# Performance work log

Measured on AMD Instinct MI355X. Metric: run time of the kernel, lower is better.

## Reference

```python
import jax, jax.numpy as jnp
import numpy as np


def setup_inputs() -> dict:
    key = jax.random.key(0)
    k1, k2, k3, k4 = jax.random.split(key, 4)
    B, N, D = 4, 2048, 1024
    scale = 1.0 / np.sqrt(D)
    return {
        "x": jax.random.normal(k1, (B, N, D), dtype=jnp.float32),
        "Wq": jax.random.normal(k2, (D, D), dtype=jnp.float32) * scale,
        "Wk": jax.random.normal(k3, (D, D), dtype=jnp.float32) * scale,
        "Wv": jax.random.normal(k4, (D, D), dtype=jnp.float32) * scale,
    }


def reference(x, Wq, Wk, Wv):
    # x: [b, n, d_in]; W*: [d_out, d_in] (torch Linear convention y = x @ W.T)
    q = jnp.einsum("bnd,od->bno", x, Wq)
    k = jnp.einsum("bnd,od->bno", x, Wk)
    v = jnp.einsum("bnd,od->bno", x, Wv)
    n = x.shape[1]
    d_out = k.shape[-1]
    scores = jnp.einsum("bqd,bkd->bqk", q, k)  # [b, n, n]
    causal = jnp.triu(jnp.ones((n, n), dtype=bool), k=1)  # True above diagonal
    scores = jnp.where(causal[None, :, :], -jnp.inf, scores)
    # NOTE: faithful to source -- softmax over dim=1 (query axis), not dim=-1
    attn = jax.nn.softmax(scores / jnp.sqrt(jnp.float32(d_out)), axis=1)
    # dropout p=0.0 (eval): identity
    return jnp.einsum("bqk,bkd->bqd", attn, v)
```

## Files before the change

kernel.cpp:

```cpp
#include <hip/hip_runtime.h>
#include <stdint.h>
#include <math.h>


typedef __attribute__((ext_vector_type(8))) short short8;
typedef __attribute__((ext_vector_type(4))) float f32x4;

static __device__ __forceinline__ ushort f2bf(float f) {
  union { float f; uint32_t u; } v; v.f = f;
  uint32_t r = v.u + 0x7FFFu + ((v.u >> 16) & 1u);
  return (ushort)(r >> 16);
}
static __device__ __forceinline__ float bf2f(ushort u) {
  union { uint32_t u; float f; } v; v.u = ((uint32_t)u) << 16;
  return v.f;
}

static __device__ __forceinline__ void gload_lds16(const ushort* g, ushort* l) {
  __builtin_amdgcn_global_load_lds(
      (const __attribute__((address_space(1))) void*)g,
      (__attribute__((address_space(3))) void*)l, 16, 0, 0);
}

#define SBAR()   __builtin_amdgcn_s_barrier()
#define SCHED0() __builtin_amdgcn_sched_barrier(0)
#define WAITL0() do { asm volatile("s_waitcnt lgkmcnt(0)" ::: "memory"); SCHED0(); } while (0)
#define WAITV3() asm volatile("s_waitcnt vmcnt(3)" ::: "memory")
#define WAITV2() asm volatile("s_waitcnt vmcnt(2)" ::: "memory")
#define WAITV0() asm volatile("s_waitcnt vmcnt(0)" ::: "memory")

__global__ void cast_all(const float* __restrict__ x, const float* __restrict__ Wq,
                         const float* __restrict__ Wk, const float* __restrict__ Wv,
                         ushort* __restrict__ xb, ushort* __restrict__ Wb,
                         int n_x4, int n_w4) {
  int i = blockIdx.x * blockDim.x + threadIdx.x;
  const float* src; ushort* dst; int off;
  if (i < n_x4) { src = x; dst = xb; off = i; }
  else {
    int j = i - n_x4;
    int z = j / n_w4;
    off = j - z * n_w4;
    src = (z == 0) ? Wq : (z == 1) ? Wk : Wv;
    dst = Wb + (long)z * n_w4 * 4;
  }
  float4 v = ((const float4*)src)[off];
  ushort4 o;
  o.x = f2bf(v.x); o.y = f2bf(v.y); o.z = f2bf(v.z); o.w = f2bf(v.w);
  ((ushort4*)dst)[off] = o;
}

__global__ __launch_bounds__(512, 4) void proj_all(
    const ushort* __restrict__ xb, const ushort* __restrict__ Wb,
    ushort* __restrict__ QK, ushort* __restrict__ Vt)
{
  const int D = 1024;
  const long BND = 8388608;
  int L = blockIdx.x;
  L = (L & 7) * 96 + (L >> 3);

  const ushort* Ab; const ushort* Bb;
  int bm0, bn0;
  if (L < 512) {
    int rem = L & 255;
    bm0 = (rem >> 3) * 256;
    bn0 = (rem & 7) * 128;
    Ab = xb;
    Bb = Wb + (long)(L >> 8) * D * D;
  } else {
    int rem = L - 512;
    bm0 = (rem >> 6) * 256;
    bn0 = (rem & 63) * 128;
    Ab = Wb + 2L * D * D;
    Bb = xb;
  }

  const int nk = 32;

  __shared__ uint4 lds_v[73728 / 16];
  char* lds = (char*)lds_v;

  const int tid  = threadIdx.x;
  const int lane = tid & 63;
  const int wave = tid >> 6;
  const int wr   = wave >> 1;
  const int wc   = wave & 1;
  const int fr   = lane & 15;
  const int fg   = lane >> 4;

  f32x4 acc[4][4];
#pragma unroll
  for (int i = 0; i < 4; ++i)
#pragma unroll
    for (int j = 0; j < 4; ++j) acc[i][j] = (f32x4){0.f, 0.f, 0.f, 0.f};

  auto STAGE = [&](int tt) {
    if (tt >= nk) return;
    char* slab = lds + (tt % 3) * 24576;
#pragma unroll
    for (int u = 0; u < 2; ++u) {
      int s = u * 512 + tid;
      int row = s >> 2;
      int cc = (s & 3) ^ ((row >> 1) & 3);
      gload_lds16(Ab + (long)(bm0 + row) * D + tt * 32 + cc * 8,
                  (ushort*)(slab + s * 16));
    }
    {
      int s = tid;
      int row = s >> 2;
      int cc = (s & 3) ^ ((row >> 1) & 3);
      gload_lds16(Bb + (long)(bn0 + row) * D + tt * 32 + cc * 8,
                  (ushort*)(slab + 16384 + s * 16));
    }
  };

  STAGE(0); STAGE(1);
  WAITV3();
  SBAR();

  for (int t = 0; t < nk; ++t) {
    char* slab = lds + (t % 3) * 24576;
    STAGE(t + 2);

    short8 a[4], b[4];
#pragma unroll
    for (int i = 0; i < 4; ++i) {
      int row = wr * 64 + i * 16 + fr;
      int cc = fg ^ ((row >> 1) & 3);
      a[i] = *(const short8*)(slab + row * 64 + cc * 16);
    }
#pragma unroll
    for (int j = 0; j < 4; ++j) {
      int row = wc * 64 + j * 16 + fr;
      int cc = fg ^ ((row >> 1) & 3);
      b[j] = *(const short8*)(slab + 16384 + row * 64 + cc * 16);
    }
    WAITL0();
    __builtin_amdgcn_s_setprio(1);
#pragma unroll
    for (int i = 0; i < 4; ++i)
#pragma unroll
      for (int j = 0; j < 4; ++j)
        acc[i][j] = __builtin_amdgcn_mfma_f32_16x16x32_bf16(a[i], b[j], acc[i][j], 0, 0, 0);
    __builtin_amdgcn_s_setprio(0);

    if (t + 2 < nk) { WAITV3(); } else { WAITV0(); }
    SBAR();
  }

  if (L < 512) {
    ushort* Cb = QK + (long)(L >> 8) * BND;
#pragma unroll
    for (int i = 0; i < 4; ++i)
#pragma unroll
      for (int j = 0; j < 4; ++j)
#pragma unroll
        for (int r = 0; r < 4; ++r) {
          int row = bm0 + wr * 64 + i * 16 + fg * 4 + r;
          int col = bn0 + wc * 64 + j * 16 + fr;
          Cb[(long)row * D + col] = f2bf(acc[i][j][r]);
        }
  } else {
    ushort* Cb = Vt + (long)(bn0 >> 11) * D * 2048;
#pragma unroll
    for (int i = 0; i < 4; ++i)
#pragma unroll
      for (int j = 0; j < 4; ++j)
#pragma unroll
        for (int r = 0; r < 4; ++r) {
          int row = bm0 + wr * 64 + i * 16 + fg * 4 + r;
          int col = (bn0 + wc * 64 + j * 16 + fr) & 2047;
          Cb[(long)row * 2048 + col] = f2bf(acc[i][j][r]);
        }
  }
}

__global__ __launch_bounds__(512, 4) void gemm_s(
    const ushort* __restrict__ Q, const ushort* __restrict__ Kb, ushort* __restrict__ S,
    float* __restrict__ pMg, float* __restrict__ pZg)
{
  const int NQ = 2048, D = 1024;
  int bid = blockIdx.x;
  bid = (bid & 7) * 68 + (bid >> 3);
  const int b = bid / 136;
  int t = bid - b * 136;
  int i = (int)((sqrtf(8.f * t + 1.f) - 1.f) * 0.5f);
  while ((i + 1) * (i + 2) / 2 <= t) ++i;
  while (i * (i + 1) / 2 > t) --i;
  const int j = t - i * (i + 1) / 2;
  const int bm0 = i * 128;
  const int bn0 = j * 128;

  const ushort* Ab = Q + (long)b * NQ * D;
  const ushort* Bb = Kb + (long)b * NQ * D;

  const int nk = 32;

  __shared__ uint4 lds_v[49152 / 16];
  char* lds = (char*)lds_v;

  const int tid  = threadIdx.x;
  const int lane = tid & 63;
  const int wave = tid >> 6;
  const int wr   = wave >> 2;
  const int wc   = wave & 3;
  const int fr   = lane & 15;
  const int fg   = lane >> 4;

  f32x4 acc[4][2];
#pragma unroll
  for (int ii = 0; ii < 4; ++ii)
#pragma unroll
    for (int jj = 0; jj < 2; ++jj) acc[ii][jj] = (f32x4){0.f, 0.f, 0.f, 0.f};

  auto STAGE = [&](int tt) {
    if (tt >= nk) return;
    char* slab = lds + (tt % 3) * 16384;
    {
      int s = tid;
      int row = s >> 2;
      int cc = (s & 3) ^ ((row >> 1) & 3);
      gload_lds16(Ab + (long)(bm0 + row) * D + tt * 32 + cc * 8,
                  (ushort*)(slab + s * 16));
    }
    {
      int s = tid;
      int row = s >> 2;
      int cc = (s & 3) ^ ((row >> 1) & 3);
      gload_lds16(Bb + (long)(bn0 + row) * D + tt * 32 + cc * 8,
                  (ushort*)(slab + 8192 + s * 16));
    }
  };

  STAGE(0); STAGE(1);
  WAITV2();
  SBAR();

  for (int tt = 0; tt < nk; ++tt) {
    char* slab = lds + (tt % 3) * 16384;
    STAGE(tt + 2);

    short8 a[4], bf[2];
#pragma unroll
    for (int ii = 0; ii < 4; ++ii) {
      int row = wr * 64 + ii * 16 + fr;
      int cc = fg ^ ((row >> 1) & 3);
      a[ii] = *(const short8*)(slab + row * 64 + cc * 16);
    }
#pragma unroll
    for (int jj = 0; jj < 2; ++jj) {
      int row = wc * 32 + jj * 16 + fr;
      int cc = fg ^ ((row >> 1) & 3);
      bf[jj] = *(const short8*)(slab + 8192 + row * 64 + cc * 16);
    }
    WAITL0();
    __builtin_amdgcn_s_setprio(1);
#pragma unroll
    for (int ii = 0; ii < 4; ++ii)
#pragma unroll
      for (int jj = 0; jj < 2; ++jj)
        acc[ii][jj] = __builtin_amdgcn_mfma_f32_16x16x32_bf16(a[ii], bf[jj], acc[ii][jj], 0, 0, 0);
    __builtin_amdgcn_s_setprio(0);

    if (tt + 2 < nk) { WAITV2(); } else { WAITV0(); }
    SBAR();
  }

  ushort* Cb = S + (long)b * NQ * NQ;
  float mcol[2];
#pragma unroll
  for (int jj = 0; jj < 2; ++jj) {
    const int colg = bn0 + wc * 32 + jj * 16 + fr;
    float m = -3.0e38f;
#pragma unroll
    for (int ii = 0; ii < 4; ++ii)
#pragma unroll
      for (int r = 0; r < 4; ++r) {
        int rowg = bm0 + wr * 64 + ii * 16 + fg * 4 + r;
        float v = acc[ii][jj][r] * 0.03125f;
        acc[ii][jj][r] = v;
        Cb[(long)rowg * NQ + colg] = f2bf(v);
        m = (rowg >= colg) ? fmaxf(m, v) : m;
      }
    m = fmaxf(m, __shfl_xor(m, 16));
    m = fmaxf(m, __shfl_xor(m, 32));
    mcol[jj] = m;
  }
  float* red = (float*)lds;
  if (fg == 0) {
    red[wr * 128 + wc * 32 + fr]      = mcol[0];
    red[wr * 128 + wc * 32 + 16 + fr] = mcol[1];
  }
  SBAR();
  float Mf[2], zcol[2];
#pragma unroll
  for (int jj = 0; jj < 2; ++jj) {
    const int c = wc * 32 + jj * 16 + fr;
    Mf[jj] = fmaxf(red[c], red[128 + c]);
    const int colg = bn0 + c;
    float z = 0.f;
#pragma unroll
    for (int ii = 0; ii < 4; ++ii)
#pragma unroll
      for (int r = 0; r < 4; ++r) {
        int rowg = bm0 + wr * 64 + ii * 16 + fg * 4 + r;
        z += (rowg >= colg) ? __expf(acc[ii][jj][r] - Mf[jj]) : 0.f;
      }
    z += __shfl_xor(z, 16);
    z += __shfl_xor(z, 32);
    zcol[jj] = z;
  }
  if (fg == 0) {
    red[256 + wr * 128 + wc * 32 + fr]      = zcol[0];
    red[256 + wr * 128 + wc * 32 + 16 + fr] = zcol[1];
  }
  SBAR();
  if (wr == 0 && fg == 0) {
#pragma unroll
    for (int jj = 0; jj < 2; ++jj) {
      const int c = wc * 32 + jj * 16 + fr;
      long o = ((long)b * 16 + i) * NQ + bn0 + c;
      pMg[o] = Mf[jj];
      pZg[o] = red[256 + c] + red[256 + 128 + c];
    }
  }
}

__global__ void colstats_combine(const float* __restrict__ pM, const float* __restrict__ pZ,
                                 float2* __restrict__ Mz, int Nq) {
  int idx = blockIdx.x * 256 + threadIdx.x;
  int b = idx / Nq, k = idx - b * Nq;
  const int i0 = k >> 7;
  const float* PM = pM + (long)b * 16 * Nq + k;
  const float* PZ = pZ + (long)b * 16 * Nq + k;
  float M = -3.0e38f;
  for (int c = i0; c < 16; ++c) M = fmaxf(M, PM[(long)c * Nq]);
  float Z = 0.f;
  for (int c = i0; c < 16; ++c) Z += PZ[(long)c * Nq] * __expf(PM[(long)c * Nq] - M);
  Mz[idx] = make_float2(M, 1.0f / Z);
}

__global__ void make_p(ushort* __restrict__ S, const float2* __restrict__ Mz, int Nq) {
  long t = (long)blockIdx.x * 256 + threadIdx.x;
  int kb = (int)(t % (Nq / 8)) * 8;
  long row = t / (Nq / 8);
  int q = (int)(row % Nq);
  int b = (int)(row / Nq);
  int kend = ((q >> 7) + 1) << 7;
  if (kb >= kend) return;
  ushort* Sp = S + row * Nq + kb;
  union { uint4 v; ushort u[8]; } d, o;
  d.v = *(const uint4*)Sp;
  const float2* mz = Mz + (long)b * Nq + kb;
#pragma unroll
  for (int j = 0; j < 8; ++j) {
    float2 m = mz[j];
    float p = (q >= kb + j) ? __expf(bf2f(d.u[j]) - m.x) * m.y : 0.f;
    o.u[j] = f2bf(p);
  }
  *(uint4*)Sp = o.v;
}

__global__ __launch_bounds__(512, 4) void gemm_pv(
    const ushort* __restrict__ P, const ushort* __restrict__ Vt, float* __restrict__ out)
{
  const int NQ = 2048, DD = 1024;
  int L = blockIdx.x;
  L = (L & 7) * 64 + (L >> 3);
  const int pr = L & 7, dt = (L >> 3) & 15, b = L >> 7;

  const ushort* Pb = P + (long)b * NQ * NQ;
  const ushort* Vb = Vt + (long)b * DD * NQ + (long)(dt * 64) * NQ;
  float* Ob = out + (long)b * NQ * DD;

  __shared__ uint4 lds_v[73728 / 16];
  char* lds = (char*)lds_v;

  const int tid  = threadIdx.x;
  const int lane = tid & 63;
  const int wave = tid >> 6;
  const int wr   = wave >> 1;
  const int wc   = wave & 1;
  const int fr   = lane & 15;
  const int fg   = lane >> 4;

  for (int h = 0; h < 2; ++h) {
    const int tq = h ? (15 - pr) : pr;
    const int q0 = tq * 128;
    const ushort* Aq = Pb + (long)q0 * NQ;
    const int nk = (tq + 1) * 2;

    f32x4 acc[2][2];
#pragma unroll
    for (int i = 0; i < 2; ++i)
#pragma unroll
      for (int j = 0; j < 2; ++j) acc[i][j] = (f32x4){0.f, 0.f, 0.f, 0.f};

    auto STAGE = [&](int tt) {
      if (tt >= nk) return;
      char* slab = lds + (tt % 3) * 24576;
#pragma unroll
      for (int u = 0; u < 2; ++u) {
        int s = u * 512 + tid;
        int row = s >> 3;
        int cc = (s & 7) ^ (row & 7);
        gload_lds16(Aq + (long)row * NQ + tt * 64 + cc * 8,
                    (ushort*)(slab + s * 16));
      }
      {
        int s = tid;
        int row = s >> 3;
        int cc = (s & 7) ^ (row & 7);
        gload_lds16(Vb + (long)row * NQ + tt * 64 + cc * 8,
                    (ushort*)(slab + 16384 + s * 16));
      }
    };

    STAGE(0); STAGE(1);
    WAITV3();
    SBAR();

    for (int t = 0; t < nk; ++t) {
      char* slab = lds + (t % 3) * 24576;
      STAGE(t + 2);

#pragma unroll
      for (int kh = 0; kh < 2; ++kh) {
        short8 a[2], bfr[2];
#pragma unroll
        for (int i = 0; i < 2; ++i) {
          int row = wr * 32 + i * 16 + fr;
          int cc = (kh * 4 + fg) ^ (row & 7);
          a[i] = *(const short8*)(slab + row * 128 + cc * 16);
        }
#pragma unroll
        for (int j = 0; j < 2; ++j) {
          int row = wc * 32 + j * 16 + fr;
          int cc = (kh * 4 + fg) ^ (row & 7);
          bfr[j] = *(const short8*)(slab + 16384 + row * 128 + cc * 16);
        }
        WAITL0();
        __builtin_amdgcn_s_setprio(1);
#pragma unroll
        for (int i = 0; i < 2; ++i)
#pragma unroll
          for (int j = 0; j < 2; ++j)
            acc[i][j] = __builtin_amdgcn_mfma_f32_16x16x32_bf16(a[i], bfr[j], acc[i][j], 0, 0, 0);
        __builtin_amdgcn_s_setprio(0);
      }

      if (t + 2 < nk) { WAITV3(); } else { WAITV0(); }
      SBAR();
    }

#pragma unroll
    for (int i = 0; i < 2; ++i)
#pragma unroll
      for (int j = 0; j < 2; ++j)
#pragma unroll
        for (int r = 0; r < 4; ++r) {
          int row = q0 + wr * 32 + i * 16 + fg * 4 + r;
          int col = dt * 64 + wc * 32 + j * 16 + fr;
          Ob[(long)row * DD + col] = acc[i][j][r];
        }
  }
}

extern "C" void kernel_launch(void* const* d_in, const int* in_sizes, int n_in,
                              void* d_out, int out_size, void* d_ws, size_t ws_size,
                              hipStream_t stream) {
  const float* x  = (const float*)d_in[0];
  const float* Wq = (const float*)d_in[1];
  const float* Wk = (const float*)d_in[2];
  const float* Wv = (const float*)d_in[3];
  float* out = (float*)d_out;

  const int B = 4, N = 2048, D = 1024;
  const long BND = (long)B * N * D;

  char* ws = (char*)d_ws;
  ushort* xb  = (ushort*)ws;
  ushort* Wb  = xb + BND;
  ushort* QK  = Wb + 3L * D * D;
  ushort* Qb  = QK;
  ushort* Kb  = QK + BND;
  ushort* Vt  = QK + 2 * BND;
  ushort* S   = Vt + BND;
  float*  pM  = (float*)(S + (long)B * N * N);
  float*  pZ  = pM + (long)B * 16 * N;
  float2* Mz  = (float2*)(pZ + (long)B * 16 * N);

  {
    int n_x4 = (int)(BND / 4);
    int n_w4 = D * D / 4;
    int total = n_x4 + 3 * n_w4;
    cast_all<<<total / 256, 256, 0, stream>>>(x, Wq, Wk, Wv, xb, Wb, n_x4, n_w4);
  }

  proj_all<<<768, 512, 0, stream>>>(xb, Wb, QK, Vt);

  gemm_s<<<544, 512, 0, stream>>>(Qb, Kb, S, pM, pZ);

  colstats_combine<<<(B * N) / 256, 256, 0, stream>>>(pM, pZ, Mz, N);

  make_p<<<(int)((long)B * N * N / 8 / 256), 256, 0, stream>>>(S, Mz, N);

  gemm_pv<<<512, 512, 0, stream>>>(S, Vt, out);
}
```

Baseline: 159.0 us.

## Fold softmax column normalization into V and store exp scores directly

```diff
diff --git a/kernel.cpp b/kernel.cpp
--- a/kernel.cpp
+++ b/kernel.cpp
@@ -25,8 +25,8 @@
 #define SBAR()   __builtin_amdgcn_s_barrier()
 #define SCHED0() __builtin_amdgcn_sched_barrier(0)
 #define WAITL0() do { asm volatile("s_waitcnt lgkmcnt(0)" ::: "memory"); SCHED0(); } while (0)
+#define WAITV4() asm volatile("s_waitcnt vmcnt(4)" ::: "memory")
 #define WAITV3() asm volatile("s_waitcnt vmcnt(3)" ::: "memory")
-#define WAITV2() asm volatile("s_waitcnt vmcnt(2)" ::: "memory")
 #define WAITV0() asm volatile("s_waitcnt vmcnt(0)" ::: "memory")
 
 __global__ void cast_all(const float* __restrict__ x, const float* __restrict__ Wq,
@@ -174,7 +174,7 @@
   }
 }
 
-__global__ __launch_bounds__(512, 4) void gemm_s(
+__global__ __launch_bounds__(256, 3) void gemm_s(
     const ushort* __restrict__ Q, const ushort* __restrict__ Kb, ushort* __restrict__ S,
     float* __restrict__ pMg, float* __restrict__ pZg)
 {
@@ -201,29 +201,31 @@
   const int tid  = threadIdx.x;
   const int lane = tid & 63;
   const int wave = tid >> 6;
-  const int wr   = wave >> 2;
-  const int wc   = wave & 3;
+  const int wr   = wave >> 1;
+  const int wc   = wave & 1;
   const int fr   = lane & 15;
   const int fg   = lane >> 4;
 
-  f32x4 acc[4][2];
+  f32x4 acc[4][4];
 #pragma unroll
   for (int ii = 0; ii < 4; ++ii)
 #pragma unroll
-    for (int jj = 0; jj < 2; ++jj) acc[ii][jj] = (f32x4){0.f, 0.f, 0.f, 0.f};
+    for (int jj = 0; jj < 4; ++jj) acc[ii][jj] = (f32x4){0.f, 0.f, 0.f, 0.f};
 
   auto STAGE = [&](int tt) {
     if (tt >= nk) return;
     char* slab = lds + (tt % 3) * 16384;
-    {
-      int s = tid;
+#pragma unroll
+    for (int u = 0; u < 2; ++u) {
+      int s = u * 256 + tid;
       int row = s >> 2;
       int cc = (s & 3) ^ ((row >> 1) & 3);
       gload_lds16(Ab + (long)(bm0 + row) * D + tt * 32 + cc * 8,
                   (ushort*)(slab + s * 16));
     }
-    {
-      int s = tid;
+#pragma unroll
+    for (int u = 0; u < 2; ++u) {
+      int s = u * 256 + tid;
       int row = s >> 2;
       int cc = (s & 3) ^ ((row >> 1) & 3);
       gload_lds16(Bb + (long)(bn0 + row) * D + tt * 32 + cc * 8,
@@ -232,14 +234,14 @@
   };
 
   STAGE(0); STAGE(1);
-  WAITV2();
+  WAITV4();
   SBAR();
 
   for (int tt = 0; tt < nk; ++tt) {
     char* slab = lds + (tt % 3) * 16384;
     STAGE(tt + 2);
 
-    short8 a[4], bf[2];
+    short8 a[4], bf[4];
 #pragma unroll
     for (int ii = 0; ii < 4; ++ii) {
       int row = wr * 64 + ii * 16 + fr;
@@ -247,8 +249,8 @@
       a[ii] = *(const short8*)(slab + row * 64 + cc * 16);
     }
 #pragma unroll
-    for (int jj = 0; jj < 2; ++jj) {
-      int row = wc * 32 + jj * 16 + fr;
+    for (int jj = 0; jj < 4; ++jj) {
+      int row = wc * 64 + jj * 16 + fr;
       int cc = fg ^ ((row >> 1) & 3);
       bf[jj] = *(const short8*)(slab + 8192 + row * 64 + cc * 16);
     }
@@ -257,19 +259,19 @@
 #pragma unroll
     for (int ii = 0; ii < 4; ++ii)
 #pragma unroll
-      for (int jj = 0; jj < 2; ++jj)
+      for (int jj = 0; jj < 4; ++jj)
         acc[ii][jj] = __builtin_amdgcn_mfma_f32_16x16x32_bf16(a[ii], bf[jj], acc[ii][jj], 0, 0, 0);
     __builtin_amdgcn_s_setprio(0);
 
-    if (tt + 2 < nk) { WAITV2(); } else { WAITV0(); }
+    if (tt + 2 < nk) { WAITV4(); } else { WAITV0(); }
     SBAR();
   }
 
   ushort* Cb = S + (long)b * NQ * NQ;
-  float mcol[2];
-#pragma unroll
-  for (int jj = 0; jj < 2; ++jj) {
-    const int colg = bn0 + wc * 32 + jj * 16 + fr;
+  float mcol[4];
+#pragma unroll
+  for (int jj = 0; jj < 4; ++jj) {
+    const int colg = bn0 + wc * 64 + jj * 16 + fr;
     float m = -3.0e38f;
 #pragma unroll
     for (int ii = 0; ii < 4; ++ii)
@@ -278,8 +280,9 @@
         int rowg = bm0 + wr * 64 + ii * 16 + fg * 4 + r;
         float v = acc[ii][jj][r] * 0.03125f;
         acc[ii][jj][r] = v;
-        Cb[(long)rowg * NQ + colg] = f2bf(v);
-        m = (rowg >= colg) ? fmaxf(m, v) : m;
+        bool ok = rowg >= colg;
+        Cb[(long)rowg * NQ + colg] = f2bf(ok ? __expf(v) : 0.f);
+        m = ok ? fmaxf(m, v) : m;
       }
     m = fmaxf(m, __shfl_xor(m, 16));
     m = fmaxf(m, __shfl_xor(m, 32));
@@ -287,14 +290,15 @@
   }
   float* red = (float*)lds;
   if (fg == 0) {
-    red[wr * 128 + wc * 32 + fr]      = mcol[0];
-    red[wr * 128 + wc * 32 + 16 + fr] = mcol[1];
+#pragma unroll
+    for (int jj = 0; jj < 4; ++jj)
+      red[wr * 128 + wc * 64 + jj * 16 + fr] = mcol[jj];
   }
   SBAR();
-  float Mf[2], zcol[2];
-#pragma unroll
-  for (int jj = 0; jj < 2; ++jj) {
-    const int c = wc * 32 + jj * 16 + fr;
+  float Mf[4], zcol[4];
+#pragma unroll
+  for (int jj = 0; jj < 4; ++jj) {
+    const int c = wc * 64 + jj * 16 + fr;
     Mf[jj] = fmaxf(red[c], red[128 + c]);
     const int colg = bn0 + c;
     float z = 0.f;
@@ -310,14 +314,15 @@
     zcol[jj] = z;
   }
   if (fg == 0) {
-    red[256 + wr * 128 + wc * 32 + fr]      = zcol[0];
-    red[256 + wr * 128 + wc * 32 + 16 + fr] = zcol[1];
+#pragma unroll
+    for (int jj = 0; jj < 4; ++jj)
+      red[256 + wr * 128 + wc * 64 + jj * 16 + fr] = zcol[jj];
   }
   SBAR();
   if (wr == 0 && fg == 0) {
 #pragma unroll
-    for (int jj = 0; jj < 2; ++jj) {
-      const int c = wc * 32 + jj * 16 + fr;
+    for (int jj = 0; jj < 4; ++jj) {
+      const int c = wc * 64 + jj * 16 + fr;
       long o = ((long)b * 16 + i) * NQ + bn0 + c;
       pMg[o] = Mf[jj];
       pZg[o] = red[256 + c] + red[256 + 128 + c];
@@ -326,7 +331,7 @@
 }
 
 __global__ void colstats_combine(const float* __restrict__ pM, const float* __restrict__ pZ,
-                                 float2* __restrict__ Mz, int Nq) {
+                                 float* __restrict__ cvec, int Nq) {
   int idx = blockIdx.x * 256 + threadIdx.x;
   int b = idx / Nq, k = idx - b * Nq;
   const int i0 = k >> 7;
@@ -336,28 +341,22 @@
   for (int c = i0; c < 16; ++c) M = fmaxf(M, PM[(long)c * Nq]);
   float Z = 0.f;
   for (int c = i0; c < 16; ++c) Z += PZ[(long)c * Nq] * __expf(PM[(long)c * Nq] - M);
-  Mz[idx] = make_float2(M, 1.0f / Z);
-}
-
-__global__ void make_p(ushort* __restrict__ S, const float2* __restrict__ Mz, int Nq) {
+  cvec[idx] = __expf(-M) / Z;
+}
+
+__global__ void scale_vt(ushort* __restrict__ Vt, const float* __restrict__ cvec,
+                         int Nq, int Dd) {
   long t = (long)blockIdx.x * 256 + threadIdx.x;
-  int kb = (int)(t % (Nq / 8)) * 8;
-  long row = t / (Nq / 8);
-  int q = (int)(row % Nq);
-  int b = (int)(row / Nq);
-  int kend = ((q >> 7) + 1) << 7;
-  if (kb >= kend) return;
-  ushort* Sp = S + row * Nq + kb;
+  long nrow = t / (Nq / 8);
+  int nb = (int)(t % (Nq / 8)) * 8;
+  int b = (int)(nrow / Dd);
+  ushort* p = Vt + nrow * Nq + nb;
+  const float* c = cvec + (long)b * Nq + nb;
   union { uint4 v; ushort u[8]; } d, o;
-  d.v = *(const uint4*)Sp;
-  const float2* mz = Mz + (long)b * Nq + kb;
-#pragma unroll
-  for (int j = 0; j < 8; ++j) {
-    float2 m = mz[j];
-    float p = (q >= kb + j) ? __expf(bf2f(d.u[j]) - m.x) * m.y : 0.f;
-    o.u[j] = f2bf(p);
-  }
-  *(uint4*)Sp = o.v;
+  d.v = *(const uint4*)p;
+#pragma unroll
+  for (int j = 0; j < 8; ++j) o.u[j] = f2bf(bf2f(d.u[j]) * c[j]);
+  *(uint4*)p = o.v;
 }
 
 __global__ __launch_bounds__(512, 4) void gemm_pv(
@@ -487,7 +486,7 @@
   ushort* S   = Vt + BND;
   float*  pM  = (float*)(S + (long)B * N * N);
   float*  pZ  = pM + (long)B * 16 * N;
-  float2* Mz  = (float2*)(pZ + (long)B * 16 * N);
+  float*  cv  = pZ + (long)B * 16 * N;
 
   {
     int n_x4 = (int)(BND / 4);
@@ -498,11 +497,11 @@
 
   proj_all<<<768, 512, 0, stream>>>(xb, Wb, QK, Vt);
 
-  gemm_s<<<544, 512, 0, stream>>>(Qb, Kb, S, pM, pZ);
-
-  colstats_combine<<<(B * N) / 256, 256, 0, stream>>>(pM, pZ, Mz, N);
-
-  make_p<<<(int)((long)B * N * N / 8 / 256), 256, 0, stream>>>(S, Mz, N);
+  gemm_s<<<544, 256, 0, stream>>>(Qb, Kb, S, pM, pZ);
+
+  colstats_combine<<<(B * N) / 256, 256, 0, stream>>>(pM, pZ, cv, N);
+
+  scale_vt<<<(int)(BND / 8 / 256), 256, 0, stream>>>(Vt, cv, N, D);
 
   gemm_pv<<<512, 512, 0, stream>>>(S, Vt, out);
 }
```

New measurement: 149.8 us. 5.8% less time.
